# Kernel optimization log

Measured on AMD Instinct MI355X. Metric: run time of the kernel, lower is better.

## Reference

```python
import jax, jax.numpy as jnp
import numpy as np

B, N, E = 64, 256, 512   # batch, leaves (power of 2), embed_size
D, U = 512, 512          # tree_size, units (controller size == units)


def setup_inputs() -> dict:
    key = jax.random.key(0)
    ks = jax.random.split(key, 11)
    sc = lambda k, shape: jax.random.normal(k, shape, dtype=jnp.float32) * 0.05
    return {
        "inputs": jax.random.normal(ks[0], (B, N, E), dtype=jnp.float32),
        "h0": sc(ks[1], (B, U)),
        "c0": sc(ks[2], (B, U)),
        "W_t": sc(ks[3], (E, D)),          # Transformer
        "W_j": sc(ks[4], (2 * D, D)),      # Join
        "W_s": sc(ks[5], (D + U, 1)),      # Search
        "W_h": sc(ks[6], (D + U, D)),      # Write candidate
        "W_T": sc(ks[7], (D + U, 1)),      # Write gate
        "kernel": sc(ks[8], (E, 4 * U)),   # LSTM input kernel (i,f,c,o)
        "rec_kernel": sc(ks[9], (U, 4 * U)),
        "bias": jnp.zeros((4 * U,), jnp.float32),
    }


def reference(inputs, h0, c0, W_t, W_j, W_s, W_h, W_T, kernel, rec_kernel, bias):
    b, n, e = inputs.shape
    control = h0  # control = previous LSTM hidden state

    # --- leaf embed: Transformer, batched over all leaves ---
    leaf_h = jax.nn.relu(jnp.einsum('bne,ed->bnd', inputs, W_t))  # [B,N,D]

    # --- refresh: bottom-up join, batched per tree level ---
    levels = [leaf_h]
    h = leaf_h
    while h.shape[1] > 1:
        pair = jnp.concatenate([h[:, 0::2], h[:, 1::2]], axis=-1)  # [B,m/2,2D]
        h = jax.nn.relu(jnp.einsum('bmk,kd->bmd', pair, W_j))
        levels.append(h)

    # --- retrieve: top-down search producing leaf attentions ---
    # Searches all use refresh-time h (parent search happens before any
    # update in its subtree), so a level-batched top-down pass is exact.
    attn = jnp.ones((b, 1, 1), inputs.dtype)
    for lvl in range(len(levels) - 1, 0, -1):
        node_h = levels[lvl]                     # [B,m,D]
        m = node_h.shape[1]
        ctrl = jnp.broadcast_to(control[:, None, :], (b, m, control.shape[-1]))
        mr = jax.nn.sigmoid(jnp.einsum('bmk,ko->bmo',
                                       jnp.concatenate([node_h, ctrl], -1), W_s))  # [B,m,1]
        # children interleave: left gets attn*(1-mr), right gets attn*mr
        attn = jnp.concatenate([attn * (1.0 - mr), attn * mr], axis=-1).reshape(b, 2 * m, 1)

    tree_out = jnp.sum(attn * inputs, axis=1)  # [B,E] soft-retrieved leaf value

    # --- write update of leaf memories, batched over all leaves ---
    ctrl = jnp.broadcast_to(control[:, None, :], (b, n, control.shape[-1]))
    data = jnp.concatenate([leaf_h, ctrl], -1)                     # [B,N,D+U]
    cand = jax.nn.sigmoid(jnp.einsum('bnk,kd->bnd', data, W_h))
    upd = jax.nn.sigmoid(jnp.einsum('bnk,ko->bno', data, W_T))
    written = upd * cand + (1.0 - upd) * leaf_h
    leaf_h_new = attn * written + (1.0 - attn) * leaf_h            # [B,N,D]

    # --- LSTM cell update (keras LSTMCell gate order i,f,c,o) ---
    z = tree_out @ kernel + h0 @ rec_kernel + bias
    zi, zf, zg, zo = jnp.split(z, 4, axis=-1)
    c_new = jax.nn.sigmoid(zf) * c0 + jax.nn.sigmoid(zi) * jnp.tanh(zg)
    h_new = jax.nn.sigmoid(zo) * jnp.tanh(c_new)
    return h_new, c_new, leaf_h_new
```

## Files before the change

### kernel.cpp

```cpp
#include <hip/hip_runtime.h>
#include <hip/hip_bf16.h>
#include <cstdint>
#include <cstddef>


__device__ __forceinline__ float sigmoidf_(float x) { return 1.0f / (1.0f + __expf(-x)); }

typedef __attribute__((ext_vector_type(8))) short bf16x8;
typedef __attribute__((ext_vector_type(4))) float f32x4;

__device__ __forceinline__ void load_lds16(const void* g, void* l) {
  __builtin_amdgcn_global_load_lds((const __attribute__((address_space(1))) void*)g,
                                   (__attribute__((address_space(3))) void*)l, 16, 0, 0);
}

__global__ __launch_bounds__(256)
void cvt_inputs(const float* __restrict__ in, __hip_bfloat16* __restrict__ outp) {
  const size_t i = ((size_t)blockIdx.x * 256 + threadIdx.x) * 8;
  float4 v0 = *(const float4*)(in + i);
  float4 v1 = *(const float4*)(in + i + 4);
  union { __hip_bfloat16 h[8]; bf16x8 v; } u;
  u.h[0] = __float2bfloat16(v0.x); u.h[1] = __float2bfloat16(v0.y);
  u.h[2] = __float2bfloat16(v0.z); u.h[3] = __float2bfloat16(v0.w);
  u.h[4] = __float2bfloat16(v1.x); u.h[5] = __float2bfloat16(v1.y);
  u.h[6] = __float2bfloat16(v1.z); u.h[7] = __float2bfloat16(v1.w);
  *(bf16x8*)(outp + i) = u.v;
}

__global__ __launch_bounds__(256)
void tconv_all(const float* __restrict__ W_t, const float* __restrict__ W_j,
               const float* __restrict__ W_h,
               __hip_bfloat16* __restrict__ Wt_t, __hip_bfloat16* __restrict__ Wt_j,
               __hip_bfloat16* __restrict__ Wt_h) {
  const int z = blockIdx.z;
  if (z != 1 && blockIdx.x >= 16) return;
  const int K = (z == 1) ? 1024 : 512;
  const float* W = (z == 0) ? W_t : ((z == 1) ? W_j : W_h);
  __hip_bfloat16* Wt = (z == 0) ? Wt_t : ((z == 1) ? Wt_j : Wt_h);
  __shared__ float sh[32][33];
  const int tx = threadIdx.x & 31, ty = threadIdx.x >> 5;
  const int k0 = blockIdx.x * 32, n0 = blockIdx.y * 32;
#pragma unroll
  for (int i = 0; i < 4; ++i)
    sh[ty + i * 8][tx] = W[(size_t)(k0 + ty + i * 8) * 512 + n0 + tx];
  __syncthreads();
#pragma unroll
  for (int i = 0; i < 4; ++i)
    Wt[(size_t)(n0 + ty + i * 8) * K + k0 + tx] = __float2bfloat16(sh[tx][ty + i * 8]);
}

template<int MODE, bool AFP32>
__global__ __launch_bounds__(256)
void mfma_gemm(const __hip_bfloat16* __restrict__ A, const float* __restrict__ Af,
               const __hip_bfloat16* __restrict__ Bt, int M, int K,
               __hip_bfloat16* __restrict__ Cb, float* __restrict__ Cf,
               const float* __restrict__ ctrl_h, const float* __restrict__ attn,
               const float* __restrict__ upd, const __hip_bfloat16* __restrict__ leaf) {
  __shared__ __align__(16) __hip_bfloat16 Asm[128 * 32];
  __shared__ __align__(16) __hip_bfloat16 Bsm[128 * 32];
  const int tid = threadIdx.x;
  const int wave = tid >> 6, lane = tid & 63;
  const int bm = blockIdx.x * 128, bn = blockIdx.y * 128;
  const int wm = (wave >> 1) * 64, wn = (wave & 1) * 64;
  const int q = lane >> 4, lr = lane & 15;

  f32x4 acc[4][4] = {};

  const int c0 = wave * 128 + lane, c1 = c0 + 64;
  const size_t ga0 = (size_t)(bm + (c0 >> 2)) * K + (c0 & 3) * 8;
  const size_t ga1 = (size_t)(bm + (c1 >> 2)) * K + (c1 & 3) * 8;
  const size_t gb0 = (size_t)(bn + (c0 >> 2)) * K + (c0 & 3) * 8;
  const size_t gb1 = (size_t)(bn + (c1 >> 2)) * K + (c1 & 3) * 8;
  __hip_bfloat16* la0 = Asm + wave * 1024;
  __hip_bfloat16* la1 = Asm + wave * 1024 + 512;
  __hip_bfloat16* lb0 = Bsm + wave * 1024;
  __hip_bfloat16* lb1 = Bsm + wave * 1024 + 512;

  for (int k0v = 0; k0v < K; k0v += 32) {
    if (AFP32) {
#pragma unroll
      for (int it = 0; it < 4; ++it) {
        const int c = it * 256 + tid;
        const int row = c >> 3, kc = c & 7;
        float4 v = *(const float4*)(Af + (size_t)(bm + row) * K + k0v + kc * 4);
        __hip_bfloat16 h[4] = {__float2bfloat16(v.x), __float2bfloat16(v.y),
                               __float2bfloat16(v.z), __float2bfloat16(v.w)};
        *(ushort4*)(Asm + row * 32 + kc * 4) = *(ushort4*)h;
      }
    } else {
      load_lds16(A + ga0 + k0v, la0);
      load_lds16(A + ga1 + k0v, la1);
    }
    load_lds16(Bt + gb0 + k0v, lb0);
    load_lds16(Bt + gb1 + k0v, lb1);
    __syncthreads();
    bf16x8 af[4], bfr[4];
#pragma unroll
    for (int mt = 0; mt < 4; ++mt)
      af[mt] = *(const bf16x8*)(Asm + (wm + mt * 16 + lr) * 32 + q * 8);
#pragma unroll
    for (int nt = 0; nt < 4; ++nt)
      bfr[nt] = *(const bf16x8*)(Bsm + (wn + nt * 16 + lr) * 32 + q * 8);
#pragma unroll
    for (int mt = 0; mt < 4; ++mt)
#pragma unroll
      for (int nt = 0; nt < 4; ++nt)
        acc[mt][nt] = __builtin_amdgcn_mfma_f32_16x16x32_bf16(af[mt], bfr[nt], acc[mt][nt], 0, 0, 0);
    __syncthreads();
  }

  if (MODE == 0) {
#pragma unroll
    for (int mt = 0; mt < 4; ++mt) {
      const int rbase = bm + wm + mt * 16 + q * 4;
#pragma unroll
      for (int nt = 0; nt < 4; ++nt) {
        const int col = bn + wn + nt * 16 + lr;
#pragma unroll
        for (int r = 0; r < 4; ++r) {
          const int row = rbase + r;
          if (row < M)
            Cb[(size_t)row * 512 + col] = __float2bfloat16(fmaxf(acc[mt][nt][r], 0.f));
        }
      }
    }
  } else {
#pragma unroll
    for (int mt = 0; mt < 4; ++mt) {
      const int rbase = bm + wm + mt * 16 + q * 4;
#pragma unroll
      for (int r = 0; r < 4; ++r) {
        const int row = rbase + r;
        const float a = attn[row];
        const float u = upd[row];
        const int bidx = row >> 8;
#pragma unroll
        for (int nt = 0; nt < 4; ++nt) {
          const int col = bn + wn + nt * 16 + lr;
          const float cand = sigmoidf_(acc[mt][nt][r] + ctrl_h[(size_t)bidx * 512 + col]);
          const float lf = __bfloat162float(leaf[(size_t)row * 512 + col]);
          const float w = u * cand + (1.f - u) * lf;
          Cf[(size_t)row * 512 + col] = a * w + (1.f - a) * lf;
        }
      }
    }
  }
}

__global__ __launch_bounds__(256)
void join_level(const __hip_bfloat16* __restrict__ in, __hip_bfloat16* __restrict__ outp,
                const __hip_bfloat16* __restrict__ Wt_j) {
  const int wave = threadIdx.x >> 6, lane = threadIdx.x & 63;
  const int q = lane >> 4, lr = lane & 15;
  const int tile = blockIdx.x * 4 + wave;
  const int mtile = tile >> 5, ntile = tile & 31;
  const __hip_bfloat16* ap = in + (size_t)(mtile * 16 + lr) * 1024 + q * 8;
  const __hip_bfloat16* bp = Wt_j + (size_t)(ntile * 16 + lr) * 1024 + q * 8;
  f32x4 acc = {0.f, 0.f, 0.f, 0.f};
#pragma unroll 8
  for (int k0 = 0; k0 < 1024; k0 += 32) {
    bf16x8 a  = *(const bf16x8*)(ap + k0);
    bf16x8 bb = *(const bf16x8*)(bp + k0);
    acc = __builtin_amdgcn_mfma_f32_16x16x32_bf16(a, bb, acc, 0, 0, 0);
  }
  const int col = ntile * 16 + lr;
  const int orow = mtile * 16 + q * 4;
#pragma unroll
  for (int r = 0; r < 4; ++r)
    outp[(size_t)(orow + r) * 512 + col] = __float2bfloat16(fmaxf(acc[r], 0.f));
}

__global__ __launch_bounds__(256)
void gemv_dual(const __hip_bfloat16* __restrict__ leaf,
               const __hip_bfloat16* __restrict__ levels,
               const float* __restrict__ W_T, const float* __restrict__ W_s,
               const float* __restrict__ ctrlT,
               float* __restrict__ upd, float* __restrict__ sc) {
  const int wave = threadIdx.x >> 6, lane = threadIdx.x & 63;
  const int bid = blockIdx.x;
  const bool is_upd = bid < 4096;
  const int row = (is_upd ? bid : (bid - 4096)) * 4 + wave;
  const __hip_bfloat16* X = is_upd ? leaf : levels;
  const float* w = is_upd ? W_T : W_s;
  union { bf16x8 v; __hip_bfloat16 e[8]; } u;
  u.v = *(const bf16x8*)(X + (size_t)row * 512 + lane * 8);
  const float* wp = w + lane * 8;
  float p = 0.f;
#pragma unroll
  for (int j = 0; j < 8; ++j) p += __bfloat162float(u.e[j]) * wp[j];
#pragma unroll
  for (int off = 32; off > 0; off >>= 1) p += __shfl_down(p, off);
  if (lane == 0) {
    if (is_upd) upd[row] = sigmoidf_(p + ctrlT[row >> 8]);
    else        sc[row] = p;
  }
}

__global__ __launch_bounds__(256)
void prep_ctrl(const float* __restrict__ h0, const float* __restrict__ W_T,
               float* __restrict__ ctrlT) {
  const int b = blockIdx.x, tid = threadIdx.x;
  __shared__ float part[256];
  float p = 0.f;
  for (int i = tid; i < 512; i += 256) p += h0[b * 512 + i] * W_T[512 + i];
  part[tid] = p; __syncthreads();
  for (int s = 128; s > 0; s >>= 1) { if (tid < s) part[tid] += part[tid + s]; __syncthreads(); }
  if (tid == 0) ctrlT[b] = part[0];
}

__global__ __launch_bounds__(256)
void propagate(const float* __restrict__ sc, const float* __restrict__ h0,
               const float* __restrict__ W_s, float* __restrict__ attn_out) {
  const int b = blockIdx.x, tid = threadIdx.x;
  __shared__ float part[256], attn_sh[256], newattn[256];
  __shared__ float scs;
  float p = 0.f;
  for (int i = tid; i < 512; i += 256) p += h0[b * 512 + i] * W_s[512 + i];
  part[tid] = p; __syncthreads();
  for (int s = 128; s > 0; s >>= 1) { if (tid < s) part[tid] += part[tid + s]; __syncthreads(); }
  if (tid == 0) { scs = part[0]; attn_sh[0] = 1.f; }
  __syncthreads();
  const int row_off[9] = {0, 0, 8192, 12288, 14336, 15360, 15872, 16128, 16256};
#pragma unroll
  for (int l = 8; l >= 1; --l) {
    const int m = 256 >> l;
    if (tid < m) {
      const float mr = sigmoidf_(sc[row_off[l] + b * m + tid] + scs);
      const float a = attn_sh[tid];
      newattn[2 * tid]     = a * (1.f - mr);
      newattn[2 * tid + 1] = a * mr;
    }
    __syncthreads();
    if (tid < 2 * m) attn_sh[tid] = newattn[tid];
    __syncthreads();
  }
  attn_out[b * 256 + tid] = attn_sh[tid];
}

__global__ __launch_bounds__(256)
void tree_part(const float* __restrict__ inputs, const float* __restrict__ attn,
               float* __restrict__ tp) {
  const int s = blockIdx.x, b = blockIdx.y;
  const int tid = threadIdx.x;
  __shared__ float a_sh[64];
  if (tid < 64) a_sh[tid] = attn[b * 256 + s * 64 + tid];
  __syncthreads();
  float acc0 = 0.f, acc1 = 0.f;
  const float* base = inputs + ((size_t)b * 256 + s * 64) * 512;
  for (int nn = 0; nn < 64; ++nn) {
    const float a = a_sh[nn];
    const float* row = base + (size_t)nn * 512;
    acc0 += a * row[tid];
    acc1 += a * row[tid + 256];
  }
  tp[((size_t)s * 64 + b) * 512 + tid]       = acc0;
  tp[((size_t)s * 64 + b) * 512 + tid + 256] = acc1;
}

__global__ __launch_bounds__(256)
void ctrl_full(const float* __restrict__ h0, const float* __restrict__ W_h,
               float* __restrict__ ch) {
  const int b = blockIdx.y;
  const int col = blockIdx.x * 256 + threadIdx.x;
  __shared__ float hsh[512];
  hsh[threadIdx.x]       = h0[b * 512 + threadIdx.x];
  hsh[threadIdx.x + 256] = h0[b * 512 + 256 + threadIdx.x];
  __syncthreads();
  const float* Wp = W_h + (size_t)512 * 512 + col;
  float s = 0.f;
#pragma unroll 8
  for (int k = 0; k < 512; ++k) s += hsh[k] * Wp[(size_t)k * 512];
  ch[(size_t)b * 512 + col] = s;
}

__global__ __launch_bounds__(256)
void lstm_gemm_splitk(const float* __restrict__ tp, const float* __restrict__ h0,
                      const float* __restrict__ kern, const float* __restrict__ rec,
                      float* __restrict__ Zp) {
  const int tid = threadIdx.x;
  const int col = blockIdx.x * 256 + tid;
  const int b0 = blockIdx.y * 4;
  const int z = blockIdx.z;
  const float* W = (z < 4) ? (kern + (size_t)z * 128 * 2048)
                           : (rec + (size_t)(z - 4) * 128 * 2048);
  const int koff = (z & 3) * 128;
  __shared__ float xs[4][128];
  for (int i = tid; i < 512; i += 256) {
    int bb = i >> 7, k = i & 127;
    const size_t idx = (size_t)(b0 + bb) * 512 + koff + k;
    float x;
    if (z < 4) x = tp[idx] + tp[32768 + idx] + tp[65536 + idx] + tp[98304 + idx];
    else       x = h0[idx];
    xs[bb][k] = x;
  }
  __syncthreads();
  float a0 = 0.f, a1 = 0.f, a2 = 0.f, a3 = 0.f;
#pragma unroll 8
  for (int k = 0; k < 128; ++k) {
    const float w = W[(size_t)k * 2048 + col];
    a0 += xs[0][k] * w;
    a1 += xs[1][k] * w;
    a2 += xs[2][k] * w;
    a3 += xs[3][k] * w;
  }
  Zp[((size_t)z * 64 + b0 + 0) * 2048 + col] = a0;
  Zp[((size_t)z * 64 + b0 + 1) * 2048 + col] = a1;
  Zp[((size_t)z * 64 + b0 + 2) * 2048 + col] = a2;
  Zp[((size_t)z * 64 + b0 + 3) * 2048 + col] = a3;
}

__global__ __launch_bounds__(256)
void lstm_combine(const float* __restrict__ Zp, const float* __restrict__ bias,
                  const float* __restrict__ c0,
                  float* __restrict__ out_h, float* __restrict__ out_c) {
  const int i = blockIdx.x * 256 + threadIdx.x;
  const int b = i >> 9, u = i & 511;
  float zi = bias[u], zf = bias[512 + u], zg = bias[1024 + u], zo = bias[1536 + u];
#pragma unroll
  for (int z = 0; z < 8; ++z) {
    const size_t base = ((size_t)z * 64 + b) * 2048;
    zi += Zp[base + u];
    zf += Zp[base + 512 + u];
    zg += Zp[base + 1024 + u];
    zo += Zp[base + 1536 + u];
  }
  const float c = sigmoidf_(zf) * c0[i] + sigmoidf_(zi) * tanhf(zg);
  out_h[i] = sigmoidf_(zo) * tanhf(c);
  out_c[i] = c;
}

extern "C" void kernel_launch(void* const* d_in, const int* in_sizes, int n_in,
                              void* d_out, int out_size, void* d_ws, size_t ws_size,
                              hipStream_t stream) {
  const float* inputs = (const float*)d_in[0];
  const float* h0     = (const float*)d_in[1];
  const float* c0     = (const float*)d_in[2];
  const float* W_t    = (const float*)d_in[3];
  const float* W_j    = (const float*)d_in[4];
  const float* W_s    = (const float*)d_in[5];
  const float* W_h    = (const float*)d_in[6];
  const float* W_T    = (const float*)d_in[7];
  const float* kern   = (const float*)d_in[8];
  const float* rec    = (const float*)d_in[9];
  const float* bias   = (const float*)d_in[10];
  float* out = (float*)d_out;

  char* p = (char*)d_ws;
  __hip_bfloat16* leaf_bf   = (__hip_bfloat16*)p; p += 16777216;
  __hip_bfloat16* levels_bf = (__hip_bfloat16*)p; p += 16842752;
  __hip_bfloat16* Wt_t      = (__hip_bfloat16*)p; p += 524288;
  __hip_bfloat16* Wt_j      = (__hip_bfloat16*)p; p += 1048576;
  __hip_bfloat16* Wt_h      = (__hip_bfloat16*)p; p += 524288;
  float* attn  = (float*)p; p += 65536;
  float* upd   = (float*)p; p += 65536;
  float* ch    = (float*)p; p += 131072;
  float* Zp    = (float*)p; p += 4194304;
  float* sc    = (float*)p; p += 65536;
  float* ctrlT = (float*)p; p += 4096;
  float* tp    = (float*)p; p += 524288;
  const bool use_cvt = ws_size >= (size_t)(p - (char*)d_ws) + 16777216;
  __hip_bfloat16* inputs_bf = (__hip_bfloat16*)p;

  tconv_all<<<dim3(32, 16, 3), 256, 0, stream>>>(W_t, W_j, W_h, Wt_t, Wt_j, Wt_h);
  ctrl_full<<<dim3(2, 64), 256, 0, stream>>>(h0, W_h, ch);
  prep_ctrl<<<64, 256, 0, stream>>>(h0, W_T, ctrlT);

  if (use_cvt) {
    cvt_inputs<<<4096, 256, 0, stream>>>(inputs, inputs_bf);
    mfma_gemm<0, false><<<dim3(128, 4), 256, 0, stream>>>(
        inputs_bf, nullptr, Wt_t, 16384, 512,
        leaf_bf, nullptr, nullptr, nullptr, nullptr, nullptr);
  } else {
    mfma_gemm<0, true><<<dim3(128, 4), 256, 0, stream>>>(
        nullptr, inputs, Wt_t, 16384, 512,
        leaf_bf, nullptr, nullptr, nullptr, nullptr, nullptr);
  }

  const int lvl_off_h[9] = {0, 0, 4194304, 6291456, 7340032,
                            7864320, 8126464, 8257536, 8323072};
  const __hip_bfloat16* Aptr = leaf_bf;
  for (int l = 1; l <= 3; ++l) {
    const int M = 64 * (256 >> l);
    __hip_bfloat16* Cl = levels_bf + lvl_off_h[l];
    mfma_gemm<0, false><<<dim3(M / 128, 4), 256, 0, stream>>>(
        Aptr, nullptr, Wt_j, M, 1024,
        Cl, nullptr, nullptr, nullptr, nullptr, nullptr);
    Aptr = Cl;
  }
  for (int l = 4; l <= 8; ++l) {
    const int m_out = 256 >> l;
    join_level<<<32 * m_out, 256, 0, stream>>>(levels_bf + lvl_off_h[l - 1],
                                               levels_bf + lvl_off_h[l], Wt_j);
  }

  gemv_dual<<<8176, 256, 0, stream>>>(leaf_bf, levels_bf, W_T, W_s, ctrlT, upd, sc);
  propagate<<<64, 256, 0, stream>>>(sc, h0, W_s, attn);

  tree_part<<<dim3(4, 64), 256, 0, stream>>>(inputs, attn, tp);

  mfma_gemm<1, false><<<dim3(128, 4), 256, 0, stream>>>(
      leaf_bf, nullptr, Wt_h, 16384, 512,
      nullptr, out + 65536, ch, attn, upd, leaf_bf);
  lstm_gemm_splitk<<<dim3(8, 16, 8), 256, 0, stream>>>(tp, h0, kern, rec, Zp);
  lstm_combine<<<128, 256, 0, stream>>>(Zp, bias, c0, out, out + 32768);
}
```

Measured before the change: 336.3 us.

## Double-buffer GEMM LDS, fuse tree tail joins, search scoring and LSTM kernels

```diff
diff --git a/kernel.cpp b/kernel.cpp
--- a/kernel.cpp
+++ b/kernel.cpp
@@ -56,8 +56,8 @@
                __hip_bfloat16* __restrict__ Cb, float* __restrict__ Cf,
                const float* __restrict__ ctrl_h, const float* __restrict__ attn,
                const float* __restrict__ upd, const __hip_bfloat16* __restrict__ leaf) {
-  __shared__ __align__(16) __hip_bfloat16 Asm[128 * 32];
-  __shared__ __align__(16) __hip_bfloat16 Bsm[128 * 32];
+  __shared__ __align__(16) __hip_bfloat16 Asm[2][128 * 32];
+  __shared__ __align__(16) __hip_bfloat16 Bsm[2][128 * 32];
   const int tid = threadIdx.x;
   const int wave = tid >> 6, lane = tid & 63;
   const int bm = blockIdx.x * 128, bn = blockIdx.y * 128;
@@ -71,13 +71,9 @@
   const size_t ga1 = (size_t)(bm + (c1 >> 2)) * K + (c1 & 3) * 8;
   const size_t gb0 = (size_t)(bn + (c0 >> 2)) * K + (c0 & 3) * 8;
   const size_t gb1 = (size_t)(bn + (c1 >> 2)) * K + (c1 & 3) * 8;
-  __hip_bfloat16* la0 = Asm + wave * 1024;
-  __hip_bfloat16* la1 = Asm + wave * 1024 + 512;
-  __hip_bfloat16* lb0 = Bsm + wave * 1024;
-  __hip_bfloat16* lb1 = Bsm + wave * 1024 + 512;
-
-  for (int k0v = 0; k0v < K; k0v += 32) {
-    if (AFP32) {
+
+  if constexpr (AFP32) {
+    for (int k0v = 0; k0v < K; k0v += 32) {
 #pragma unroll
       for (int it = 0; it < 4; ++it) {
         const int c = it * 256 + tid;
@@ -85,28 +81,52 @@
         float4 v = *(const float4*)(Af + (size_t)(bm + row) * K + k0v + kc * 4);
         __hip_bfloat16 h[4] = {__float2bfloat16(v.x), __float2bfloat16(v.y),
                                __float2bfloat16(v.z), __float2bfloat16(v.w)};
-        *(ushort4*)(Asm + row * 32 + kc * 4) = *(ushort4*)h;
-      }
-    } else {
-      load_lds16(A + ga0 + k0v, la0);
-      load_lds16(A + ga1 + k0v, la1);
-    }
-    load_lds16(Bt + gb0 + k0v, lb0);
-    load_lds16(Bt + gb1 + k0v, lb1);
-    __syncthreads();
-    bf16x8 af[4], bfr[4];
-#pragma unroll
-    for (int mt = 0; mt < 4; ++mt)
-      af[mt] = *(const bf16x8*)(Asm + (wm + mt * 16 + lr) * 32 + q * 8);
-#pragma unroll
-    for (int nt = 0; nt < 4; ++nt)
-      bfr[nt] = *(const bf16x8*)(Bsm + (wn + nt * 16 + lr) * 32 + q * 8);
-#pragma unroll
-    for (int mt = 0; mt < 4; ++mt)
+        *(ushort4*)(Asm[0] + row * 32 + kc * 4) = *(ushort4*)h;
+      }
+      load_lds16(Bt + gb0 + k0v, Bsm[0] + wave * 1024);
+      load_lds16(Bt + gb1 + k0v, Bsm[0] + wave * 1024 + 512);
+      __syncthreads();
+      bf16x8 af[4], bfr[4];
+#pragma unroll
+      for (int mt = 0; mt < 4; ++mt)
+        af[mt] = *(const bf16x8*)(Asm[0] + (wm + mt * 16 + lr) * 32 + q * 8);
 #pragma unroll
       for (int nt = 0; nt < 4; ++nt)
-        acc[mt][nt] = __builtin_amdgcn_mfma_f32_16x16x32_bf16(af[mt], bfr[nt], acc[mt][nt], 0, 0, 0);
-    __syncthreads();
+        bfr[nt] = *(const bf16x8*)(Bsm[0] + (wn + nt * 16 + lr) * 32 + q * 8);
+#pragma unroll
+      for (int mt = 0; mt < 4; ++mt)
+#pragma unroll
+        for (int nt = 0; nt < 4; ++nt)
+          acc[mt][nt] = __builtin_amdgcn_mfma_f32_16x16x32_bf16(af[mt], bfr[nt], acc[mt][nt], 0, 0, 0);
+      __syncthreads();
+    }
+  } else {
+    auto stage = [&](int s, int kv) {
+      load_lds16(A + ga0 + kv, Asm[s] + wave * 1024);
+      load_lds16(A + ga1 + kv, Asm[s] + wave * 1024 + 512);
+      load_lds16(Bt + gb0 + kv, Bsm[s] + wave * 1024);
+      load_lds16(Bt + gb1 + kv, Bsm[s] + wave * 1024 + 512);
+    };
+    stage(0, 0);
+    __syncthreads();
+    int cur = 0;
+    for (int kv = 0; kv < K; kv += 32) {
+      if (kv + 32 < K) stage(cur ^ 1, kv + 32);
+      bf16x8 af[4], bfr[4];
+#pragma unroll
+      for (int mt = 0; mt < 4; ++mt)
+        af[mt] = *(const bf16x8*)(Asm[cur] + (wm + mt * 16 + lr) * 32 + q * 8);
+#pragma unroll
+      for (int nt = 0; nt < 4; ++nt)
+        bfr[nt] = *(const bf16x8*)(Bsm[cur] + (wn + nt * 16 + lr) * 32 + q * 8);
+#pragma unroll
+      for (int mt = 0; mt < 4; ++mt)
+#pragma unroll
+        for (int nt = 0; nt < 4; ++nt)
+          acc[mt][nt] = __builtin_amdgcn_mfma_f32_16x16x32_bf16(af[mt], bfr[nt], acc[mt][nt], 0, 0, 0);
+      __syncthreads();
+      cur ^= 1;
+    }
   }
 
   if (MODE == 0) {
@@ -148,84 +168,144 @@
 }
 
 __global__ __launch_bounds__(256)
-void join_level(const __hip_bfloat16* __restrict__ in, __hip_bfloat16* __restrict__ outp,
-                const __hip_bfloat16* __restrict__ Wt_j) {
+void join_tail(__hip_bfloat16* __restrict__ levels, const __hip_bfloat16* __restrict__ Wt_j) {
+  const int b = blockIdx.x;
+  const int tid = threadIdx.x;
+  const int wave = tid >> 6, lane = tid & 63;
+  const int q = lane >> 4, lr = lane & 15;
+  __shared__ __align__(16) __hip_bfloat16 cur[32 * 512];
+  {
+    const __hip_bfloat16* src = levels + 6291456 + (size_t)b * 32 * 512;
+    for (int i = tid; i < 2048; i += 256) {
+      const int row = i >> 6, c8 = (i & 63) * 8;
+      const int byte = ((row * 512 + c8) * 2) ^ ((row & 7) << 4);
+      *(bf16x8*)((char*)cur + byte) = *(const bf16x8*)(src + row * 512 + c8);
+    }
+  }
+  __syncthreads();
+  const int out_off[5] = {7340032, 7864320, 8126464, 8257536, 8323072};
+  int m_out = 16;
+#pragma unroll
+  for (int l = 0; l < 5; ++l) {
+    f32x4 acc[8];
+#pragma unroll
+    for (int nt = 0; nt < 8; ++nt) acc[nt] = f32x4{0.f, 0.f, 0.f, 0.f};
+    for (int k0 = 0; k0 < 1024; k0 += 32) {
+      const int k = k0 + q * 8;
+      const int r2 = 2 * lr + (k >> 9);
+      const int byte = ((r2 * 512 + (k & 511)) * 2) ^ ((r2 & 7) << 4);
+      bf16x8 af = *(const bf16x8*)((const char*)cur + byte);
+#pragma unroll
+      for (int nt = 0; nt < 8; ++nt) {
+        const int brow = (wave * 8 + nt) * 16 + lr;
+        bf16x8 bb = *(const bf16x8*)(Wt_j + (size_t)brow * 1024 + k);
+        acc[nt] = __builtin_amdgcn_mfma_f32_16x16x32_bf16(af, bb, acc[nt], 0, 0, 0);
+      }
+    }
+    __syncthreads();
+    __hip_bfloat16* gout = levels + out_off[l] + (size_t)b * m_out * 512;
+#pragma unroll
+    for (int nt = 0; nt < 8; ++nt) {
+      const int col = (wave * 8 + nt) * 16 + lr;
+#pragma unroll
+      for (int r = 0; r < 4; ++r) {
+        const int row = q * 4 + r;
+        const __hip_bfloat16 v = __float2bfloat16(fmaxf(acc[nt][r], 0.f));
+        const int byte = ((row * 512 + col) * 2) ^ ((row & 7) << 4);
+        *(__hip_bfloat16*)((char*)cur + byte) = v;
+        if (row < m_out) gout[(size_t)row * 512 + col] = v;
+      }
+    }
+    __syncthreads();
+    m_out >>= 1;
+  }
+}
+
+__global__ __launch_bounds__(256)
+void gemv_upd(const __hip_bfloat16* __restrict__ leaf, const float* __restrict__ W_T,
+              const float* __restrict__ ctrlT, float* __restrict__ upd) {
   const int wave = threadIdx.x >> 6, lane = threadIdx.x & 63;
-  const int q = lane >> 4, lr = lane & 15;
-  const int tile = blockIdx.x * 4 + wave;
-  const int mtile = tile >> 5, ntile = tile & 31;
-  const __hip_bfloat16* ap = in + (size_t)(mtile * 16 + lr) * 1024 + q * 8;
-  const __hip_bfloat16* bp = Wt_j + (size_t)(ntile * 16 + lr) * 1024 + q * 8;
-  f32x4 acc = {0.f, 0.f, 0.f, 0.f};
+  const int row = blockIdx.x * 4 + wave;
+  union { bf16x8 v; __hip_bfloat16 e[8]; } u;
+  u.v = *(const bf16x8*)(leaf + (size_t)row * 512 + lane * 8);
+  const float* wp = W_T + lane * 8;
+  float p = 0.f;
+#pragma unroll
+  for (int j = 0; j < 8; ++j) p += __bfloat162float(u.e[j]) * wp[j];
+#pragma unroll
+  for (int off = 32; off > 0; off >>= 1) p += __shfl_down(p, off);
+  if (lane == 0) upd[row] = sigmoidf_(p + ctrlT[row >> 8]);
+}
+
+__global__ __launch_bounds__(256)
+void ctrl_prep(const float* __restrict__ h0, const float* __restrict__ W_h,
+               const float* __restrict__ W_T, float* __restrict__ ch,
+               float* __restrict__ ctrlT) {
+  const int b = blockIdx.y, tid = threadIdx.x;
+  if (blockIdx.x == 2) {
+    __shared__ float part[256];
+    float p = 0.f;
+    for (int i = tid; i < 512; i += 256) p += h0[b * 512 + i] * W_T[512 + i];
+    part[tid] = p; __syncthreads();
+    for (int s = 128; s > 0; s >>= 1) { if (tid < s) part[tid] += part[tid + s]; __syncthreads(); }
+    if (tid == 0) ctrlT[b] = part[0];
+  } else {
+    __shared__ float hsh[512];
+    hsh[tid]       = h0[b * 512 + tid];
+    hsh[tid + 256] = h0[b * 512 + 256 + tid];
+    __syncthreads();
+    const int col = blockIdx.x * 256 + tid;
+    const float* Wp = W_h + (size_t)512 * 512 + col;
+    float s = 0.f;
 #pragma unroll 8
-  for (int k0 = 0; k0 < 1024; k0 += 32) {
-    bf16x8 a  = *(const bf16x8*)(ap + k0);
-    bf16x8 bb = *(const bf16x8*)(bp + k0);
-    acc = __builtin_amdgcn_mfma_f32_16x16x32_bf16(a, bb, acc, 0, 0, 0);
-  }
-  const int col = ntile * 16 + lr;
-  const int orow = mtile * 16 + q * 4;
-#pragma unroll
-  for (int r = 0; r < 4; ++r)
-    outp[(size_t)(orow + r) * 512 + col] = __float2bfloat16(fmaxf(acc[r], 0.f));
-}
-
-__global__ __launch_bounds__(256)
-void gemv_dual(const __hip_bfloat16* __restrict__ leaf,
-               const __hip_bfloat16* __restrict__ levels,
-               const float* __restrict__ W_T, const float* __restrict__ W_s,
-               const float* __restrict__ ctrlT,
-               float* __restrict__ upd, float* __restrict__ sc) {
-  const int wave = threadIdx.x >> 6, lane = threadIdx.x & 63;
-  const int bid = blockIdx.x;
-  const bool is_upd = bid < 4096;
-  const int row = (is_upd ? bid : (bid - 4096)) * 4 + wave;
-  const __hip_bfloat16* X = is_upd ? leaf : levels;
-  const float* w = is_upd ? W_T : W_s;
-  union { bf16x8 v; __hip_bfloat16 e[8]; } u;
-  u.v = *(const bf16x8*)(X + (size_t)row * 512 + lane * 8);
-  const float* wp = w + lane * 8;
-  float p = 0.f;
-#pragma unroll
-  for (int j = 0; j < 8; ++j) p += __bfloat162float(u.e[j]) * wp[j];
-#pragma unroll
-  for (int off = 32; off > 0; off >>= 1) p += __shfl_down(p, off);
-  if (lane == 0) {
-    if (is_upd) upd[row] = sigmoidf_(p + ctrlT[row >> 8]);
-    else        sc[row] = p;
-  }
-}
-
-__global__ __launch_bounds__(256)
-void prep_ctrl(const float* __restrict__ h0, const float* __restrict__ W_T,
-               float* __restrict__ ctrlT) {
+    for (int k = 0; k < 512; ++k) s += hsh[k] * Wp[(size_t)k * 512];
+    ch[(size_t)b * 512 + col] = s;
+  }
+}
+
+__global__ __launch_bounds__(256)
+void propagate_sc(const __hip_bfloat16* __restrict__ levels, const float* __restrict__ h0,
+                  const float* __restrict__ W_s, float* __restrict__ attn_out) {
   const int b = blockIdx.x, tid = threadIdx.x;
-  __shared__ float part[256];
-  float p = 0.f;
-  for (int i = tid; i < 512; i += 256) p += h0[b * 512 + i] * W_T[512 + i];
-  part[tid] = p; __syncthreads();
-  for (int s = 128; s > 0; s >>= 1) { if (tid < s) part[tid] += part[tid + s]; __syncthreads(); }
-  if (tid == 0) ctrlT[b] = part[0];
-}
-
-__global__ __launch_bounds__(256)
-void propagate(const float* __restrict__ sc, const float* __restrict__ h0,
-               const float* __restrict__ W_s, float* __restrict__ attn_out) {
-  const int b = blockIdx.x, tid = threadIdx.x;
-  __shared__ float part[256], attn_sh[256], newattn[256];
-  __shared__ float scs;
+  const int wave = tid >> 6, lane = tid & 63;
+  __shared__ float part[256], ws[512], sc_sh[256], attn_sh[256], newattn[256];
+  __shared__ float scs_sh;
+  ws[tid] = W_s[tid]; ws[tid + 256] = W_s[tid + 256];
   float p = 0.f;
   for (int i = tid; i < 512; i += 256) p += h0[b * 512 + i] * W_s[512 + i];
   part[tid] = p; __syncthreads();
   for (int s = 128; s > 0; s >>= 1) { if (tid < s) part[tid] += part[tid + s]; __syncthreads(); }
-  if (tid == 0) { scs = part[0]; attn_sh[0] = 1.f; }
-  __syncthreads();
-  const int row_off[9] = {0, 0, 8192, 12288, 14336, 15360, 15872, 16128, 16256};
+  if (tid == 0) { scs_sh = part[0]; attn_sh[0] = 1.f; }
+  __syncthreads();
+  const float scs = scs_sh;
+  const int rowbase[9] = {0, 0, 8192, 12288, 14336, 15360, 15872, 16128, 16256};
+  const int nodeoff[9] = {0, 0, 128, 192, 224, 240, 248, 252, 254};
+  for (int l = 1; l <= 8; ++l) {
+    const int m = 256 >> l;
+    for (int j0 = wave * 8; j0 < m; j0 += 32) {
+      const int j = j0 + (lane >> 3), s = lane & 7;
+      float q = 0.f;
+      if (j < m) {
+        const __hip_bfloat16* xr = levels + (size_t)(rowbase[l] + b * m + j) * 512;
+#pragma unroll
+        for (int i = 0; i < 8; ++i) {
+          const int k = (i * 8 + s) * 8;
+          union { bf16x8 v; __hip_bfloat16 e[8]; } u;
+          u.v = *(const bf16x8*)(xr + k);
+#pragma unroll
+          for (int jj = 0; jj < 8; ++jj) q += __bfloat162float(u.e[jj]) * ws[k + jj];
+        }
+      }
+      q += __shfl_xor(q, 1); q += __shfl_xor(q, 2); q += __shfl_xor(q, 4);
+      if (s == 0 && j < m) sc_sh[nodeoff[l] + j] = q;
+    }
+  }
+  __syncthreads();
 #pragma unroll
   for (int l = 8; l >= 1; --l) {
     const int m = 256 >> l;
     if (tid < m) {
-      const float mr = sigmoidf_(sc[row_off[l] + b * m + tid] + scs);
+      const float mr = sigmoidf_(sc_sh[nodeoff[l] + tid] + scs);
       const float a = attn_sh[tid];
       newattn[2 * tid]     = a * (1.f - mr);
       newattn[2 * tid + 1] = a * mr;
@@ -258,75 +338,43 @@
 }
 
 __global__ __launch_bounds__(256)
-void ctrl_full(const float* __restrict__ h0, const float* __restrict__ W_h,
-               float* __restrict__ ch) {
-  const int b = blockIdx.y;
-  const int col = blockIdx.x * 256 + threadIdx.x;
-  __shared__ float hsh[512];
-  hsh[threadIdx.x]       = h0[b * 512 + threadIdx.x];
-  hsh[threadIdx.x + 256] = h0[b * 512 + 256 + threadIdx.x];
-  __syncthreads();
-  const float* Wp = W_h + (size_t)512 * 512 + col;
-  float s = 0.f;
-#pragma unroll 8
-  for (int k = 0; k < 512; ++k) s += hsh[k] * Wp[(size_t)k * 512];
-  ch[(size_t)b * 512 + col] = s;
-}
-
-__global__ __launch_bounds__(256)
-void lstm_gemm_splitk(const float* __restrict__ tp, const float* __restrict__ h0,
-                      const float* __restrict__ kern, const float* __restrict__ rec,
-                      float* __restrict__ Zp) {
+void lstm_fused(const float* __restrict__ tp, const float* __restrict__ h0,
+                const float* __restrict__ kern, const float* __restrict__ rec,
+                const float* __restrict__ bias, const float* __restrict__ c0,
+                float* __restrict__ out_h, float* __restrict__ out_c) {
   const int tid = threadIdx.x;
-  const int col = blockIdx.x * 256 + tid;
+  const int ug = tid & 63, gate = tid >> 6;
   const int b0 = blockIdx.y * 4;
-  const int z = blockIdx.z;
-  const float* W = (z < 4) ? (kern + (size_t)z * 128 * 2048)
-                           : (rec + (size_t)(z - 4) * 128 * 2048);
-  const int koff = (z & 3) * 128;
-  __shared__ float xs[4][128];
-  for (int i = tid; i < 512; i += 256) {
-    int bb = i >> 7, k = i & 127;
-    const size_t idx = (size_t)(b0 + bb) * 512 + koff + k;
-    float x;
-    if (z < 4) x = tp[idx] + tp[32768 + idx] + tp[65536 + idx] + tp[98304 + idx];
-    else       x = h0[idx];
-    xs[bb][k] = x;
-  }
-  __syncthreads();
-  float a0 = 0.f, a1 = 0.f, a2 = 0.f, a3 = 0.f;
-#pragma unroll 8
-  for (int k = 0; k < 128; ++k) {
-    const float w = W[(size_t)k * 2048 + col];
-    a0 += xs[0][k] * w;
-    a1 += xs[1][k] * w;
-    a2 += xs[2][k] * w;
-    a3 += xs[3][k] * w;
-  }
-  Zp[((size_t)z * 64 + b0 + 0) * 2048 + col] = a0;
-  Zp[((size_t)z * 64 + b0 + 1) * 2048 + col] = a1;
-  Zp[((size_t)z * 64 + b0 + 2) * 2048 + col] = a2;
-  Zp[((size_t)z * 64 + b0 + 3) * 2048 + col] = a3;
-}
-
-__global__ __launch_bounds__(256)
-void lstm_combine(const float* __restrict__ Zp, const float* __restrict__ bias,
-                  const float* __restrict__ c0,
-                  float* __restrict__ out_h, float* __restrict__ out_c) {
-  const int i = blockIdx.x * 256 + threadIdx.x;
-  const int b = i >> 9, u = i & 511;
-  float zi = bias[u], zf = bias[512 + u], zg = bias[1024 + u], zo = bias[1536 + u];
-#pragma unroll
-  for (int z = 0; z < 8; ++z) {
-    const size_t base = ((size_t)z * 64 + b) * 2048;
-    zi += Zp[base + u];
-    zf += Zp[base + 512 + u];
-    zg += Zp[base + 1024 + u];
-    zo += Zp[base + 1536 + u];
-  }
-  const float c = sigmoidf_(zf) * c0[i] + sigmoidf_(zi) * tanhf(zg);
-  out_h[i] = sigmoidf_(zo) * tanhf(c);
-  out_c[i] = c;
+  __shared__ float xs[4][512], hs[4][512];
+  for (int i = tid; i < 2048; i += 256) {
+    const int bb = i >> 9, k = i & 511;
+    const size_t idx = (size_t)(b0 + bb) * 512 + k;
+    xs[bb][k] = tp[idx] + tp[32768 + idx] + tp[65536 + idx] + tp[98304 + idx];
+    hs[bb][k] = h0[idx];
+  }
+  __syncthreads();
+  const int col = gate * 512 + blockIdx.x * 64 + ug;
+  float a0 = bias[col], a1 = a0, a2 = a0, a3 = a0;
+#pragma unroll 4
+  for (int k = 0; k < 512; ++k) {
+    const float wk = kern[(size_t)k * 2048 + col];
+    const float wr = rec[(size_t)k * 2048 + col];
+    a0 += xs[0][k] * wk + hs[0][k] * wr;
+    a1 += xs[1][k] * wk + hs[1][k] * wr;
+    a2 += xs[2][k] * wk + hs[2][k] * wr;
+    a3 += xs[3][k] * wk + hs[3][k] * wr;
+  }
+  __shared__ float zs[4][4][64];
+  zs[gate][0][ug] = a0; zs[gate][1][ug] = a1;
+  zs[gate][2][ug] = a2; zs[gate][3][ug] = a3;
+  __syncthreads();
+  const int cb = tid >> 6, cu = tid & 63;
+  const float zi = zs[0][cb][cu], zf = zs[1][cb][cu];
+  const float zg = zs[2][cb][cu], zo = zs[3][cb][cu];
+  const int gi = (b0 + cb) * 512 + blockIdx.x * 64 + cu;
+  const float c = sigmoidf_(zf) * c0[gi] + sigmoidf_(zi) * tanhf(zg);
+  out_h[gi] = sigmoidf_(zo) * tanhf(c);
+  out_c[gi] = c;
 }
 
 extern "C" void kernel_launch(void* const* d_in, const int* in_sizes, int n_in,
@@ -354,16 +402,13 @@
   float* attn  = (float*)p; p += 65536;
   float* upd   = (float*)p; p += 65536;
   float* ch    = (float*)p; p += 131072;
-  float* Zp    = (float*)p; p += 4194304;
-  float* sc    = (float*)p; p += 65536;
   float* ctrlT = (float*)p; p += 4096;
   float* tp    = (float*)p; p += 524288;
   const bool use_cvt = ws_size >= (size_t)(p - (char*)d_ws) + 16777216;
   __hip_bfloat16* inputs_bf = (__hip_bfloat16*)p;
 
   tconv_all<<<dim3(32, 16, 3), 256, 0, stream>>>(W_t, W_j, W_h, Wt_t, Wt_j, Wt_h);
-  ctrl_full<<<dim3(2, 64), 256, 0, stream>>>(h0, W_h, ch);
-  prep_ctrl<<<64, 256, 0, stream>>>(h0, W_T, ctrlT);
+  ctrl_prep<<<dim3(3, 64), 256, 0, stream>>>(h0, W_h, W_T, ch, ctrlT);
 
   if (use_cvt) {
     cvt_inputs<<<4096, 256, 0, stream>>>(inputs, inputs_bf);
@@ -387,20 +432,16 @@
         Cl, nullptr, nullptr, nullptr, nullptr, nullptr);
     Aptr = Cl;
   }
-  for (int l = 4; l <= 8; ++l) {
-    const int m_out = 256 >> l;
-    join_level<<<32 * m_out, 256, 0, stream>>>(levels_bf + lvl_off_h[l - 1],
-                                               levels_bf + lvl_off_h[l], Wt_j);
-  }
-
-  gemv_dual<<<8176, 256, 0, stream>>>(leaf_bf, levels_bf, W_T, W_s, ctrlT, upd, sc);
-  propagate<<<64, 256, 0, stream>>>(sc, h0, W_s, attn);
+  join_tail<<<64, 256, 0, stream>>>(levels_bf, Wt_j);
+
+  gemv_upd<<<4096, 256, 0, stream>>>(leaf_bf, W_T, ctrlT, upd);
+  propagate_sc<<<64, 256, 0, stream>>>(levels_bf, h0, W_s, attn);
 
   tree_part<<<dim3(4, 64), 256, 0, stream>>>(inputs, attn, tp);
 
   mfma_gemm<1, false><<<dim3(128, 4), 256, 0, stream>>>(
       leaf_bf, nullptr, Wt_h, 16384, 512,
       nullptr, out + 65536, ch, attn, upd, leaf_bf);
-  lstm_gemm_splitk<<<dim3(8, 16, 8), 256, 0, stream>>>(tp, h0, kern, rec, Zp);
-  lstm_combine<<<128, 256, 0, stream>>>(Zp, bias, c0, out, out + 32768);
-}
+
+  lstm_fused<<<dim3(8, 16), 256, 0, stream>>>(tp, h0, kern, rec, bias, c0, out, out + 32768);
+}
```

New measurement: 490.4 us. +45.8%, slower.
